# Kernel tuning notes

Measured on AMD Instinct MI355X. Metric: run time of the kernel, lower is better.

Reference implementation:

```python
import jax, jax.numpy as jnp
import numpy as np
import math

B = 2; SEQ = 4096; D_MODEL = 768; D_STATE = 128; D_CONV = 4; EXPAND = 2; HEAD_DIM = 64
D_INNER = EXPAND * D_MODEL; D_SSM = D_INNER; NH = D_SSM // HEAD_DIM  # 24 heads
CONV_DIM = D_SSM + 2 * D_STATE; CHUNK = 256
D_IN_PROJ = 2 * D_INNER + 2 * D_STATE + NH


def causal_conv1d(x, w, b):
    # x: [B, C, L]; w: [C, W] depthwise kernel; left-pad for causality; silu activation
    W = w.shape[-1]; L = x.shape[-1]
    xp = jnp.pad(x, ((0, 0), (0, 0), (W - 1, 0)))
    y = b[None, :, None] + sum(xp[:, :, k:k + L] * w[None, :, k, None] for k in range(W))
    return jax.nn.silu(y)


def segsum(a):
    # a: [..., S] -> [..., S, S]; entry (i,j) = sum_{k=j+1..i} a_k for i>=j, -inf above diag
    S = a.shape[-1]
    cs = jnp.cumsum(a, -1)
    d = cs[..., :, None] - cs[..., None, :]
    mask = jnp.tril(jnp.ones((S, S), bool))
    return jnp.where(mask, d, -jnp.inf)


def ssd_chunk_scan(x, dt, A, Bm, Cm, Dp, chunk):
    # Mamba2 SSD chunked selective scan. x:[b,l,h,p] dt:[b,l,h] A:[h] Bm,Cm:[b,l,n] Dp:[h]
    b, l, h, p = x.shape; n = Bm.shape[-1]; nc = l // chunk
    xc = x.reshape(b, nc, chunk, h, p)
    Bc = Bm.reshape(b, nc, chunk, n)
    Cc = Cm.reshape(b, nc, chunk, n)
    dtc = dt.reshape(b, nc, chunk, h)
    a = jnp.transpose(A[None, None, None, :] * dtc, (0, 3, 1, 2))  # [b,h,c,s]
    Acs = jnp.cumsum(a, -1)
    Lm = jnp.exp(segsum(a))  # [b,h,c,s,s] lower-triangular decay
    # intra-chunk (diagonal block) outputs
    Ydiag = jnp.einsum('bcsn,bczn,bhcsz,bczh,bczhp->bcshp', Cc, Bc, Lm, dtc, xc)
    # per-chunk end states
    decay_states = jnp.exp(Acs[..., -1:] - Acs)  # [b,h,c,s]
    states = jnp.einsum('bczn,bhcz,bczh,bczhp->bchpn', Bc, decay_states, dtc, xc)
    # inter-chunk recurrence over nc chunks (small) via scan
    decay_chunk = jnp.exp(Acs[..., -1])  # [b,h,c]
    def step(hcar, inp):
        dcy, st = inp
        return dcy[..., None, None] * hcar + st, hcar  # emit state entering chunk
    _, prev = jax.lax.scan(step, jnp.zeros_like(states[:, 0]),
                           (jnp.moveaxis(decay_chunk, -1, 0), jnp.moveaxis(states, 1, 0)))
    prev = jnp.moveaxis(prev, 0, 1)  # [b,c,h,p,n]
    Yoff = jnp.einsum('bcsn,bchpn,bhcs->bcshp', Cc, prev, jnp.exp(Acs))
    return (Ydiag + Yoff).reshape(b, l, h, p) + Dp[None, None, :, None] * x


def _forward(u, time_diff, W_in, b_in, conv_w, conv_b, tconv1_w, tconv1_b,
             tconv2_w, tconv2_b, mlp_w1, mlp_b1, mlp_w2, mlp_b2, gate_w, gate_b,
             ln_w, ln_b, A_log, dt_bias, Dp, norm_w, W_out, b_out):
    silu = jax.nn.silu
    zxbcdt = u @ W_in.T + b_in  # [B,L,d_in_proj], d_mlp=0
    z = zxbcdt[..., :D_SSM]
    xBC = zxbcdt[..., D_SSM:D_SSM + CONV_DIM]
    dt = zxbcdt[..., D_SSM + CONV_DIM:]  # [B,L,H]
    A = -jnp.exp(A_log)
    xBC = jnp.transpose(causal_conv1d(jnp.transpose(xBC, (0, 2, 1)), conv_w, conv_b), (0, 2, 1))
    # time-gated dt path (time_diff: [B,H,L])
    ts = silu(time_diff @ mlp_w1.T + mlp_b1) @ mlp_w2.T + mlp_b2
    tdt = ts * time_diff
    tdt = causal_conv1d(tdt, tconv1_w, tconv1_b)
    tdt = causal_conv1d(tdt, tconv2_w, tconv2_b)  # [B,H,L]
    final_dt = dt * jnp.transpose(tdt, (0, 2, 1))
    x = xBC[..., :D_SSM]
    Bm = xBC[..., D_SSM:D_SSM + D_STATE]
    Cm = xBC[..., D_SSM + D_STATE:]
    dt_sp = jax.nn.softplus(final_dt + dt_bias)
    xh = x.reshape(x.shape[0], x.shape[1], NH, HEAD_DIM)
    y = ssd_chunk_scan(xh, dt_sp, A, Bm, Cm, Dp, CHUNK).reshape(x.shape[0], x.shape[1], D_SSM)
    # gated RMSNorm (norm_before_gate=False): gate first, then normalize
    yg = y * silu(z)
    y = yg * jax.lax.rsqrt(jnp.mean(yg * yg, -1, keepdims=True) + 1e-12) * norm_w
    out = y @ W_out.T + b_out
    # time residual gate + LayerNorm over seq_len
    tg = jax.nn.sigmoid(time_diff @ gate_w.T + gate_b)  # [B,H,1]
    tmix = tg * time_diff + (1.0 - tg) * tdt
    mu = jnp.mean(tmix, -1, keepdims=True)
    var = jnp.mean((tmix - mu) ** 2, -1, keepdims=True)
    time_out = (tmix - mu) * jax.lax.rsqrt(var + 1e-12) * ln_w + ln_b
    return out, time_out


def setup_inputs():
    key = jax.random.key(0)
    ks = jax.random.split(key, 16)
    def nrm(k, shape, scale=0.02):
        return jax.random.normal(k, shape, jnp.float32) * scale
    dtv = jnp.exp(jax.random.uniform(ks[10], (NH,), jnp.float32) * (math.log(0.1) - math.log(0.001)) + math.log(0.001))
    dtv = jnp.clip(dtv, 1e-4)
    dt_bias = dtv + jnp.log(-jnp.expm1(-dtv))
    A_log = jnp.log(jax.random.uniform(ks[11], (NH,), jnp.float32, 1.0, 16.0))
    return dict(
        u=jax.random.normal(ks[0], (B, SEQ, D_MODEL), jnp.float32),
        time_diff=jax.random.uniform(ks[1], (B, NH, SEQ), jnp.float32),
        W_in=nrm(ks[2], (D_IN_PROJ, D_MODEL)), b_in=jnp.zeros((D_IN_PROJ,), jnp.float32),
        conv_w=nrm(ks[3], (CONV_DIM, D_CONV), 0.2), conv_b=jnp.zeros((CONV_DIM,), jnp.float32),
        tconv1_w=nrm(ks[4], (NH, D_CONV), 0.2), tconv1_b=jnp.zeros((NH,), jnp.float32),
        tconv2_w=nrm(ks[5], (NH, D_CONV), 0.2), tconv2_b=jnp.zeros((NH,), jnp.float32),
        mlp_w1=nrm(ks[6], (SEQ, SEQ)), mlp_b1=jnp.zeros((SEQ,), jnp.float32),
        mlp_w2=nrm(ks[7], (SEQ, SEQ)), mlp_b2=jnp.zeros((SEQ,), jnp.float32),
        gate_w=nrm(ks[8], (1, SEQ)), gate_b=jnp.zeros((1,), jnp.float32),
        ln_w=jnp.ones((SEQ,), jnp.float32), ln_b=jnp.zeros((SEQ,), jnp.float32),
        A_log=A_log, dt_bias=dt_bias, Dp=jnp.ones((NH,), jnp.float32),
        norm_w=jnp.ones((D_SSM,), jnp.float32),
        W_out=nrm(ks[9], (D_MODEL, D_INNER)), b_out=jnp.zeros((D_MODEL,), jnp.float32),
    )


def reference(u, time_diff, W_in, b_in, conv_w, conv_b, tconv1_w, tconv1_b,
              tconv2_w, tconv2_b, mlp_w1, mlp_b1, mlp_w2, mlp_b2, gate_w, gate_b,
              ln_w, ln_b, A_log, dt_bias, Dp, norm_w, W_out, b_out):
    return _forward(u, time_diff, W_in, b_in, conv_w, conv_b, tconv1_w, tconv1_b,
                    tconv2_w, tconv2_b, mlp_w1, mlp_b1, mlp_w2, mlp_b2, gate_w, gate_b,
                    ln_w, ln_b, A_log, dt_bias, Dp, norm_w, W_out, b_out)
```

## Files before the change

kernel.cpp:

```cpp
#include <hip/hip_runtime.h>
#include <math.h>

#define BB 2
#define SEQ 4096
#define DMODEL 768
#define DSTATE 128
#define NHH 24
#define HDIM 64
#define DSSM 1536
#define CDIM 1792
#define CHK 256
#define NC 16
#define DPROJ 3352
#define MR (BB*SEQ)
#define KSPLIT 32
#define XSTR 1920
#define CT 16
#define SXS 270
#define STS 134

typedef __attribute__((ext_vector_type(8))) short bf16x8;
typedef __attribute__((ext_vector_type(8))) unsigned short u16x8;
typedef __attribute__((ext_vector_type(4))) float f32x4;

__device__ __forceinline__ float siluf(float x) { return x / (1.0f + expf(-x)); }

__device__ __forceinline__ unsigned short f2bf(float f) {
    unsigned u = __float_as_uint(f);
    unsigned r = (u + 0x7fffu + ((u >> 16) & 1u)) >> 16;
    return (unsigned short)r;
}

__device__ __forceinline__ float bf2f(unsigned short u) {
    return __uint_as_float(((unsigned)u) << 16);
}

__device__ __forceinline__ float4 bf2f4(ushort4 v) {
    float4 o;
    o.x = bf2f(v.x); o.y = bf2f(v.y); o.z = bf2f(v.z); o.w = bf2f(v.w);
    return o;
}

__device__ __forceinline__ bf16x8 pack8(float4 a, float4 b) {
    u16x8 r;
    r[0] = f2bf(a.x); r[1] = f2bf(a.y); r[2] = f2bf(a.z); r[3] = f2bf(a.w);
    r[4] = f2bf(b.x); r[5] = f2bf(b.y); r[6] = f2bf(b.z); r[7] = f2bf(b.w);
    return *(bf16x8*)&r;
}

__device__ __forceinline__ void gload_lds16(const void* g, void* l) {
    __builtin_amdgcn_global_load_lds((const __attribute__((address_space(1))) unsigned int*)g,
                                     (__attribute__((address_space(3))) unsigned int*)l, 16, 0, 0);
}

__global__ __launch_bounds__(256) void cvt_bf16_k(const float* __restrict__ in,
    unsigned short* __restrict__ out, int n_valid, int n_total)
{
    int i = (blockIdx.x * 256 + threadIdx.x) * 4;
    if (i >= n_total) return;
    ushort4 o;
    if (i + 3 < n_valid) {
        float4 v = *(const float4*)&in[i];
        o.x = f2bf(v.x); o.y = f2bf(v.y); o.z = f2bf(v.z); o.w = f2bf(v.w);
    } else {
        o.x = (i + 0 < n_valid) ? f2bf(in[i + 0]) : 0;
        o.y = (i + 1 < n_valid) ? f2bf(in[i + 1]) : 0;
        o.z = (i + 2 < n_valid) ? f2bf(in[i + 2]) : 0;
        o.w = (i + 3 < n_valid) ? f2bf(in[i + 3]) : 0;
    }
    *(ushort4*)&out[i] = o;
}

__global__ __launch_bounds__(256) void gemm_dual_skinny(
    const unsigned short* __restrict__ A,
    const unsigned short* __restrict__ B1, const float* __restrict__ bias1,
    unsigned short* __restrict__ C1, int N1, int NT1, int nbias1, int NWG1,
    const unsigned short* __restrict__ B2, const float* __restrict__ bias2,
    unsigned short* __restrict__ C2, int N2, int NT2, int nbias2,
    int K, int KT, int NWGD,
    const float* __restrict__ skA, const float* __restrict__ skB,
    float* __restrict__ skPart, int skN, int skK)
{
    __shared__ unsigned short SMEM[24576];
    const int tid = threadIdx.x;
    const int w = tid >> 6, l = tid & 63;
    const int lr = l & 15, lk = l >> 4;
    int nwg = gridDim.x, bid = blockIdx.x;
    int wg = (nwg & 7) ? bid : ((bid & 7) * (nwg >> 3) + (bid >> 3));
    if (wg >= NWGD) {
        int t = wg - NWGD;
        int nb = t & 31, kb = t >> 5;
        const int n0s = nb * 128;
        const int KS = skK / KSPLIT;
        const int k0 = kb * KS;
        const int nw0 = n0s + w * 32;
        f32x4 sacc[3][2] = {};
        for (int kt = 0; kt < KS; kt += 32) {
            int kk = k0 + kt + lk * 8;
            bf16x8 af[3], bfr[2];
#pragma unroll
            for (int mi = 0; mi < 3; ++mi) {
                const float* ap = &skA[(size_t)(mi * 16 + lr) * skK + kk];
                af[mi] = pack8(*(const float4*)ap, *(const float4*)(ap + 4));
            }
#pragma unroll
            for (int nf = 0; nf < 2; ++nf) {
                const float* bp = &skB[(size_t)(nw0 + nf * 16 + lr) * skK + kk];
                bfr[nf] = pack8(*(const float4*)bp, *(const float4*)(bp + 4));
            }
#pragma unroll
            for (int mi = 0; mi < 3; ++mi)
#pragma unroll
                for (int nf = 0; nf < 2; ++nf)
                    sacc[mi][nf] = __builtin_amdgcn_mfma_f32_16x16x32_bf16(af[mi], bfr[nf], sacc[mi][nf], 0, 0, 0);
        }
        float* pb = skPart + (size_t)kb * 48 * skN;
#pragma unroll
        for (int mi = 0; mi < 3; ++mi)
#pragma unroll
            for (int r = 0; r < 4; ++r)
#pragma unroll
                for (int nf = 0; nf < 2; ++nf)
                    pb[(size_t)(mi * 16 + lk * 4 + r) * skN + nw0 + nf * 16 + lr] = sacc[mi][nf][r];
        return;
    }
    const int wr = w >> 1, wc = w & 1;
    const int lkx = lk ^ ((lr >> 1) & 3);
    const unsigned short* B;
    const float* bias;
    unsigned short* C;
    int N, NT, nbias;
    if (wg < NWG1) { B = B1; bias = bias1; C = C1; N = N1; NT = NT1; nbias = nbias1; }
    else { wg -= NWG1; B = B2; bias = bias2; C = C2; N = N2; NT = NT2; nbias = nbias2; }
    const int m0 = (wg / NT) * 128, n0 = (wg % NT) * 128;
    f32x4 acc[4][4] = {};
    const int i16 = w * 64 + l;
    const int row0 = i16 >> 2, sl = i16 & 3;
    const int slx = sl ^ ((row0 >> 1) & 3);
    const size_t ga0 = (size_t)(m0 + row0) * K + slx * 8;
    const size_t ga1 = (size_t)(m0 + row0 + 64) * K + slx * 8;
    const size_t gb0 = (size_t)(n0 + row0) * K + slx * 8;
    const size_t gb1 = (size_t)(n0 + row0 + 64) * K + slx * 8;
    const int lo0 = (w * 64) * 8;
    const int lo1 = (256 + w * 64) * 8;

#define STAGE(bb, kt) { int ko = (kt) * 32; int bs = (bb) * 8192;            \
      gload_lds16(A + ga0 + ko, &SMEM[bs + lo0]);                            \
      gload_lds16(A + ga1 + ko, &SMEM[bs + lo1]);                            \
      gload_lds16(B + gb0 + ko, &SMEM[bs + 4096 + lo0]);                     \
      gload_lds16(B + gb1 + ko, &SMEM[bs + 4096 + lo1]); }

    STAGE(0, 0);
    STAGE(1, 1);
    for (int kt = 0; kt < KT; ++kt) {
        if (kt + 1 < KT) {
            asm volatile("s_waitcnt vmcnt(4)" ::: "memory");
        } else {
            asm volatile("s_waitcnt vmcnt(0)" ::: "memory");
        }
        __builtin_amdgcn_s_barrier();
        if (kt + 2 < KT) STAGE((kt + 2) % 3, kt + 2);
        int bs = (kt % 3) * 8192;
        bf16x8 af[4], bg[4];
#pragma unroll
        for (int mi = 0; mi < 4; ++mi)
            af[mi] = *(const bf16x8*)&SMEM[bs + (wr * 64 + mi * 16 + lr) * 32 + lkx * 8];
#pragma unroll
        for (int nj = 0; nj < 4; ++nj)
            bg[nj] = *(const bf16x8*)&SMEM[bs + 4096 + (wc * 64 + nj * 16 + lr) * 32 + lkx * 8];
#pragma unroll
        for (int mi = 0; mi < 4; ++mi)
#pragma unroll
            for (int nj = 0; nj < 4; ++nj)
                acc[mi][nj] = __builtin_amdgcn_mfma_f32_16x16x32_bf16(af[mi], bg[nj], acc[mi][nj], 0, 0, 0);
    }
#undef STAGE
    {
        unsigned short* CL = SMEM;
#pragma unroll
        for (int half = 0; half < 2; ++half) {
            __syncthreads();
            if (wr == half) {
#pragma unroll
                for (int nj = 0; nj < 4; ++nj) {
                    int col = n0 + wc * 64 + nj * 16 + lr;
                    float bz = (col < nbias) ? bias[col] : 0.f;
                    int cl = wc * 64 + nj * 16 + lr;
#pragma unroll
                    for (int mi = 0; mi < 4; ++mi)
#pragma unroll
                        for (int r = 0; r < 4; ++r)
                            CL[(mi * 16 + lk * 4 + r) * 136 + cl] = f2bf(acc[mi][nj][r] + bz);
                }
            }
            __syncthreads();
            for (int i = tid; i < 1024; i += 256) {
                int rr = i >> 4, c8 = (i & 15) * 8;
                int m = m0 + half * 64 + rr;
                *(u16x8*)&C[(size_t)m * N + n0 + c8] = *(const u16x8*)&CL[rr * 136 + c8];
            }
        }
    }
}

__global__ __launch_bounds__(256) void conv_skinny2_k(const unsigned short* __restrict__ xbc,
    const float* __restrict__ cw, const float* __restrict__ cb,
    unsigned short* __restrict__ out,
    const float* __restrict__ skA, const float* __restrict__ skB,
    float* __restrict__ skPart, int skN, int skK, int NWGC)
{
    int bid = blockIdx.x;
    int tid = threadIdx.x;
    if (bid >= NWGC) {
        int t = bid - NWGC;
        int nb = t & 31, kb = t >> 5;
        const int n0s = nb * 128;
        const int KS = skK / KSPLIT;
        const int k0 = kb * KS;
        const int w = tid >> 6, l = tid & 63;
        const int lr = l & 15, lk = l >> 4;
        const int nw0 = n0s + w * 32;
        f32x4 sacc[3][2] = {};
        for (int kt = 0; kt < KS; kt += 32) {
            int kk = k0 + kt + lk * 8;
            bf16x8 af[3], bfr[2];
#pragma unroll
            for (int mi = 0; mi < 3; ++mi) {
                const float* ap = &skA[(size_t)(mi * 16 + lr) * skK + kk];
                af[mi] = pack8(*(const float4*)ap, *(const float4*)(ap + 4));
            }
#pragma unroll
            for (int nf = 0; nf < 2; ++nf) {
                const float* bp = &skB[(size_t)(nw0 + nf * 16 + lr) * skK + kk];
                bfr[nf] = pack8(*(const float4*)bp, *(const float4*)(bp + 4));
            }
#pragma unroll
            for (int mi = 0; mi < 3; ++mi)
#pragma unroll
                for (int nf = 0; nf < 2; ++nf)
                    sacc[mi][nf] = __builtin_amdgcn_mfma_f32_16x16x32_bf16(af[mi], bfr[nf], sacc[mi][nf], 0, 0, 0);
        }
        float* pb = skPart + (size_t)kb * 48 * skN;
#pragma unroll
        for (int mi = 0; mi < 3; ++mi)
#pragma unroll
            for (int r = 0; r < 4; ++r)
#pragma unroll
                for (int nf = 0; nf < 2; ++nf)
                    pb[(size_t)(mi * 16 + lk * 4 + r) * skN + nw0 + nf * 16 + lr] = sacc[mi][nf][r];
        return;
    }
    int idx = bid * 256 + tid;
    int slot = idx % 448;
    int g = idx / 448;
    int c4 = slot * 4;
    int b = g / (SEQ / CT);
    int t0 = (g % (SEQ / CT)) * CT;
    size_t rb = (size_t)b * SEQ;
    float4 cw0 = *(const float4*)&cw[(c4 + 0) * 4];
    float4 cw1 = *(const float4*)&cw[(c4 + 1) * 4];
    float4 cw2 = *(const float4*)&cw[(c4 + 2) * 4];
    float4 cw3 = *(const float4*)&cw[(c4 + 3) * 4];
    float4 cbv = *(const float4*)&cb[c4];
    float4 zero = {0.f, 0.f, 0.f, 0.f};
    float4 w0, w1, w2;
    w0 = (t0 - 3 >= 0) ? bf2f4(*(const ushort4*)&xbc[(rb + t0 - 3) * XSTR + c4]) : zero;
    w1 = (t0 - 2 >= 0) ? bf2f4(*(const ushort4*)&xbc[(rb + t0 - 2) * XSTR + c4]) : zero;
    w2 = (t0 - 1 >= 0) ? bf2f4(*(const ushort4*)&xbc[(rb + t0 - 1) * XSTR + c4]) : zero;
#pragma unroll
    for (int i = 0; i < CT; ++i) {
        int t = t0 + i;
        float4 w3 = bf2f4(*(const ushort4*)&xbc[(rb + t) * XSTR + c4]);
        float a0 = cbv.x + w0.x * cw0.x + w1.x * cw0.y + w2.x * cw0.z + w3.x * cw0.w;
        float a1 = cbv.y + w0.y * cw1.x + w1.y * cw1.y + w2.y * cw1.z + w3.y * cw1.w;
        float a2 = cbv.z + w0.z * cw2.x + w1.z * cw2.y + w2.z * cw2.z + w3.z * cw2.w;
        float a3 = cbv.w + w0.w * cw3.x + w1.w * cw3.y + w2.w * cw3.z + w3.w * cw3.w;
        ushort4 o;
        o.x = f2bf(siluf(a0)); o.y = f2bf(siluf(a1));
        o.z = f2bf(siluf(a2)); o.w = f2bf(siluf(a3));
        *(ushort4*)&out[(rb + t) * CDIM + c4] = o;
        w0 = w1; w1 = w2; w2 = w3;
    }
}

__global__ __launch_bounds__(256) void reduce_part_k(const float* __restrict__ part,
    const float* __restrict__ bias, float* __restrict__ out, int N, int act)
{
    int idx = blockIdx.x * 256 + threadIdx.x;
    if (idx >= 48 * N) return;
    int n = idx % N;
    float s = bias[n];
#pragma unroll
    for (int kb = 0; kb < KSPLIT; ++kb) s += part[(size_t)kb * 48 * N + idx];
    if (act) s = siluf(s);
    out[idx] = s;
}

__global__ __launch_bounds__(256) void time_conv_k(const float* __restrict__ ts,
    const float* __restrict__ td, const float* __restrict__ w1, const float* __restrict__ b1,
    const float* __restrict__ w2, const float* __restrict__ b2, float* __restrict__ tdt)
{
    __shared__ float u0[SEQ];
    __shared__ float u1[SEQ];
    int row = blockIdx.x, h = row % NHH;
    const float* tsr = ts + (size_t)row * SEQ;
    const float* tdr = td + (size_t)row * SEQ;
    for (int i = threadIdx.x; i < SEQ; i += 256) u0[i] = tsr[i] * tdr[i];
    __syncthreads();
    float wa[4], wb[4];
#pragma unroll
    for (int k = 0; k < 4; ++k) { wa[k] = w1[h * 4 + k]; wb[k] = w2[h * 4 + k]; }
    float ba = b1[h], bbv = b2[h];
    for (int i = threadIdx.x; i < SEQ; i += 256) {
        float acc = ba;
#pragma unroll
        for (int k = 0; k < 4; ++k) { int tt = i + k - 3; if (tt >= 0) acc = fmaf(u0[tt], wa[k], acc); }
        u1[i] = siluf(acc);
    }
    __syncthreads();
    for (int i = threadIdx.x; i < SEQ; i += 256) {
        float acc = bbv;
#pragma unroll
        for (int k = 0; k < 4; ++k) { int tt = i + k - 3; if (tt >= 0) acc = fmaf(u1[tt], wb[k], acc); }
        tdt[(size_t)row * SEQ + i] = siluf(acc);
    }
}

__global__ __launch_bounds__(256) void dtsp_cum_k(const unsigned short* __restrict__ r1,
    const float* __restrict__ tdt, const float* __restrict__ dt_bias,
    const float* __restrict__ A_log, float* __restrict__ dtp, float* __restrict__ acs)
{
    __shared__ float wsum[4];
    int blk = blockIdx.x;
    int c = blk % NC;
    int bh = blk / NC;
    int h = bh % NHH, b = bh / NHH;
    int tid = threadIdx.x;
    int s = c * CHK + tid;
    size_t base = (size_t)bh * SEQ + s;
    float x = bf2f(r1[((size_t)(b * SEQ + s)) * XSTR + CDIM + h]) * tdt[base] + dt_bias[h];
    float dt = (x > 20.0f) ? x : log1pf(expf(x));
    dtp[base] = dt;
    float Ah = -expf(A_log[h]);
    float v = Ah * dt;
    int ln = tid & 63;
#pragma unroll
    for (int off = 1; off < 64; off <<= 1) {
        float t = __shfl_up(v, off, 64);
        if (ln >= off) v += t;
    }
    if (ln == 63) wsum[tid >> 6] = v;
    __syncthreads();
    float add = 0.f;
    int wv = tid >> 6;
#pragma unroll
    for (int i = 0; i < 3; ++i)
        if (i < wv) add += wsum[i];
    acs[base] = v + add;
}

__global__ __launch_bounds__(256) void ssd_states_sraw_k(const unsigned short* __restrict__ xc,
    const float* __restrict__ dtp, const float* __restrict__ acs_g,
    float* __restrict__ st, unsigned short* __restrict__ sraw)
{
    __shared__ float s_coef[256];
    __shared__ unsigned short SXT[64 * STS];
    __shared__ unsigned short SBT[128 * STS];
    int bid = blockIdx.x;
    int blk = (gridDim.x & 7) ? bid : ((bid & 7) * (gridDim.x >> 3) + (bid >> 3));
    int tid = threadIdx.x;
    int w = tid >> 6, l = tid & 63;
    int lr = l & 15, lk = l >> 4;
    if (blk >= BB * NC * NHH) {
        int t = blk - BB * NC * NHH;
        int bc = t / 10, tile = t % 10;
        int rem = tile, st_i = 0;
        for (st_i = 0; ; ++st_i) { if (rem < st_i + 1) break; rem -= st_i + 1; }
        int zt = rem;
        int b = bc / NC, c = bc % NC;
        size_t rowbase = (size_t)b * SEQ + c * CHK;
        for (int i = tid; i < 64 * 32; i += 256) {
            int r = i >> 5, c4 = (i & 31) * 4;
            *(ushort4*)&SXT[r * STS + c4] = *(const ushort4*)&xc[(rowbase + st_i * 64 + r) * CDIM + DSSM + DSTATE + c4];
            *(ushort4*)&SBT[r * STS + c4] = *(const ushort4*)&xc[(rowbase + zt * 64 + r) * CDIM + DSSM + c4];
        }
        __syncthreads();
        f32x4 d[4] = {};
#pragma unroll
        for (int kt = 0; kt < 4; ++kt) {
            bf16x8 av = *(const bf16x8*)&SXT[(w * 16 + lr) * STS + kt * 32 + lk * 8];
            bf16x8 bv[4];
#pragma unroll
            for (int nj = 0; nj < 4; ++nj)
                bv[nj] = *(const bf16x8*)&SBT[(nj * 16 + lr) * STS + kt * 32 + lk * 8];
#pragma unroll
            for (int nj = 0; nj < 4; ++nj)
                d[nj] = __builtin_amdgcn_mfma_f32_16x16x32_bf16(av, bv[nj], d[nj], 0, 0, 0);
        }
        unsigned short* tp = sraw + (size_t)bc * 16 * 4096 + (size_t)(st_i * 4 + zt) * 4096;
#pragma unroll
        for (int nj = 0; nj < 4; ++nj)
#pragma unroll
            for (int r = 0; r < 4; ++r)
                tp[(w * 16 + lk * 4 + r) * 64 + nj * 16 + lr] = f2bf(d[nj][r]);
        return;
    }
    int h = blk % NHH, c = (blk / NHH) % NC, b = blk / (NHH * NC);
    size_t rowbase = (size_t)b * SEQ + c * CHK;
    size_t dbase = (size_t)(b * NHH + h) * SEQ + c * CHK;
    float alv = acs_g[dbase + 255];
    s_coef[tid] = expf(alv - acs_g[dbase + tid]) * dtp[dbase + tid];
    __syncthreads();
    f32x4 acc[4][2] = {};
    for (int z0 = 0; z0 < CHK; z0 += 128) {
        if (z0) __syncthreads();
        for (int i = tid; i < 128 * 8; i += 256) {
            int zz = i >> 3, p8 = (i & 7) * 8;
            float sc = s_coef[z0 + zz];
            u16x8 v = *(const u16x8*)&xc[(rowbase + z0 + zz) * CDIM + h * HDIM + p8];
#pragma unroll
            for (int e = 0; e < 8; ++e)
                SXT[(p8 + e) * STS + zz] = f2bf(bf2f(v[e]) * sc);
        }
        for (int i = tid; i < 128 * 16; i += 256) {
            int zz = i >> 4, n8 = (i & 15) * 8;
            u16x8 v = *(const u16x8*)&xc[(rowbase + z0 + zz) * CDIM + DSSM + n8];
#pragma unroll
            for (int e = 0; e < 8; ++e)
                SBT[(n8 + e) * STS + zz] = v[e];
        }
        __syncthreads();
#pragma unroll
        for (int kt = 0; kt < 4; ++kt) {
            bf16x8 av[4], bv[2];
#pragma unroll
            for (int mi = 0; mi < 4; ++mi)
                av[mi] = *(const bf16x8*)&SXT[(mi * 16 + lr) * STS + kt * 32 + lk * 8];
#pragma unroll
            for (int nj = 0; nj < 2; ++nj)
                bv[nj] = *(const bf16x8*)&SBT[(w * 32 + nj * 16 + lr) * STS + kt * 32 + lk * 8];
#pragma unroll
            for (int mi = 0; mi < 4; ++mi)
#pragma unroll
                for (int nj = 0; nj < 2; ++nj)
                    acc[mi][nj] = __builtin_amdgcn_mfma_f32_16x16x32_bf16(av[mi], bv[nj], acc[mi][nj], 0, 0, 0);
        }
    }
    size_t base = (size_t)blk * (HDIM * DSTATE);
#pragma unroll
    for (int mi = 0; mi < 4; ++mi)
#pragma unroll
        for (int r = 0; r < 4; ++r) {
            int p = mi * 16 + lk * 4 + r;
#pragma unroll
            for (int nj = 0; nj < 2; ++nj)
                st[base + p * DSTATE + w * 32 + nj * 16 + lr] = acc[mi][nj][r];
        }
}

__global__ __launch_bounds__(256) void ssd_scan_k(const float* __restrict__ st,
    const float* __restrict__ acs_g, unsigned short* __restrict__ pv16)
{
    int b = blockIdx.x / NHH, h = blockIdx.x % NHH;
    int tid = threadIdx.x;
    float carry[32];
#pragma unroll
    for (int j = 0; j < 32; ++j) carry[j] = 0.f;
    for (int c = 0; c < NC; ++c) {
        int bch = (b * NC + c) * NHH + h;
        size_t base = (size_t)bch * (HDIM * DSTATE);
        float dcy = expf(acs_g[(size_t)(b * NHH + h) * SEQ + c * CHK + 255]);
#pragma unroll
        for (int j = 0; j < 32; ++j) {
            pv16[base + tid + j * 256] = f2bf(carry[j]);
            carry[j] = fmaf(dcy, carry[j], st[base + tid + j * 256]);
        }
    }
}

__global__ __launch_bounds__(256) void ssd_y2_k(const unsigned short* __restrict__ xc,
    const float* __restrict__ dtp, const float* __restrict__ acs_g,
    const unsigned short* __restrict__ sraw, const unsigned short* __restrict__ pv16,
    const float* __restrict__ Dp, unsigned short* __restrict__ Ybf)
{
    __shared__ unsigned short SXT[32 * SXS];
    int bid = blockIdx.x;
    int blk2 = (gridDim.x & 7) ? bid : ((bid & 7) * (gridDim.x >> 3) + (bid >> 3));
    int half = blk2 & 1;
    int blk = blk2 >> 1;
    int h = blk % NHH;
    int c = (blk / NHH) % NC;
    int b = blk / (NHH * NC);
    int tid = threadIdx.x;
    int w = tid >> 6, l = tid & 63;
    int lr = l & 15, lk = l >> 4;
    int pbase = half * 32;
    size_t rowbase = (size_t)b * SEQ + c * CHK;
    size_t dbase = (size_t)(b * NHH + h) * SEQ + c * CHK;
    for (int i = tid; i < 256 * 4; i += 256) {
        int z = i >> 2, p8 = (i & 3) * 8;
        float az0q = acs_g[dbase + (z & 192)];
        float e = az0q - acs_g[dbase + z];
        if (e > 60.f) e = 60.f;
        float sc = expf(e) * dtp[dbase + z];
        u16x8 v = *(const u16x8*)&xc[(rowbase + z) * CDIM + h * HDIM + pbase + p8];
#pragma unroll
        for (int e2 = 0; e2 < 8; ++e2)
            SXT[(p8 + e2) * SXS + z] = f2bf(bf2f(v[e2]) * sc);
    }
    float az0w = acs_g[dbase + w * 64];
    float esw[4][4];
#pragma unroll
    for (int mi = 0; mi < 4; ++mi)
#pragma unroll
        for (int r = 0; r < 4; ++r)
            esw[mi][r] = expf(acs_g[dbase + w * 64 + mi * 16 + lk * 4 + r] - az0w);
    __syncthreads();

    const unsigned short* tbase = sraw + (size_t)(b * NC + c) * 16 * 4096;
    const unsigned short* pvbase = pv16 + (size_t)blk * (HDIM * DSTATE);
    f32x4 acc[4][2] = {};
    for (int zt = 0; zt < w; ++zt) {
        const unsigned short* tp = tbase + (size_t)(w * 4 + zt) * 4096;
        f32x4 tmp[4][2] = {};
#pragma unroll
        for (int kt = 0; kt < 2; ++kt) {
            bf16x8 av[4], bv[2];
#pragma unroll
            for (int mi = 0; mi < 4; ++mi)
                av[mi] = *(const bf16x8*)&tp[(mi * 16 + lr) * 64 + kt * 32 + lk * 8];
#pragma unroll
            for (int nj = 0; nj < 2; ++nj)
                bv[nj] = *(const bf16x8*)&SXT[(nj * 16 + lr) * SXS + zt * 64 + kt * 32 + lk * 8];
#pragma unroll
            for (int mi = 0; mi < 4; ++mi)
#pragma unroll
                for (int nj = 0; nj < 2; ++nj)
                    tmp[mi][nj] = __builtin_amdgcn_mfma_f32_16x16x32_bf16(av[mi], bv[nj], tmp[mi][nj], 0, 0, 0);
        }
        float rho = expf(az0w - acs_g[dbase + zt * 64]);
#pragma unroll
        for (int mi = 0; mi < 4; ++mi)
#pragma unroll
            for (int r = 0; r < 4; ++r) {
                float es = esw[mi][r] * rho;
#pragma unroll
                for (int nj = 0; nj < 2; ++nj)
                    acc[mi][nj][r] += es * tmp[mi][nj][r];
            }
    }
    {
        const unsigned short* tp = tbase + (size_t)(w * 4 + w) * 4096;
        f32x4 tmp[4][2] = {};
#pragma unroll
        for (int kt = 0; kt < 2; ++kt) {
            bf16x8 av[4], bv[2];
#pragma unroll
            for (int mi = 0; mi < 4; ++mi) {
                av[mi] = *(const bf16x8*)&tp[(mi * 16 + lr) * 64 + kt * 32 + lk * 8];
                int zb = kt * 32 + lk * 8;
                int sl = mi * 16 + lr;
#pragma unroll
                for (int e = 0; e < 8; ++e)
                    if (zb + e > sl) av[mi][e] = 0;
            }
#pragma unroll
            for (int nj = 0; nj < 2; ++nj)
                bv[nj] = *(const bf16x8*)&SXT[(nj * 16 + lr) * SXS + w * 64 + kt * 32 + lk * 8];
#pragma unroll
            for (int mi = 0; mi < 4; ++mi)
#pragma unroll
                for (int nj = 0; nj < 2; ++nj)
                    tmp[mi][nj] = __builtin_amdgcn_mfma_f32_16x16x32_bf16(av[mi], bv[nj], tmp[mi][nj], 0, 0, 0);
        }
#pragma unroll
        for (int mi = 0; mi < 4; ++mi)
#pragma unroll
            for (int r = 0; r < 4; ++r) {
                float es = esw[mi][r];
#pragma unroll
                for (int nj = 0; nj < 2; ++nj)
                    acc[mi][nj][r] += es * tmp[mi][nj][r];
            }
    }
    {
        f32x4 tmp[4][2] = {};
#pragma unroll
        for (int kt = 0; kt < 4; ++kt) {
            bf16x8 av[4], bv[2];
#pragma unroll
            for (int mi = 0; mi < 4; ++mi)
                av[mi] = *(const bf16x8*)&xc[(rowbase + w * 64 + mi * 16 + lr) * CDIM + DSSM + DSTATE + kt * 32 + lk * 8];
#pragma unroll
            for (int nj = 0; nj < 2; ++nj)
                bv[nj] = *(const bf16x8*)&pvbase[(pbase + nj * 16 + lr) * DSTATE + kt * 32 + lk * 8];
#pragma unroll
            for (int mi = 0; mi < 4; ++mi)
#pragma unroll
                for (int nj = 0; nj < 2; ++nj)
                    tmp[mi][nj] = __builtin_amdgcn_mfma_f32_16x16x32_bf16(av[mi], bv[nj], tmp[mi][nj], 0, 0, 0);
        }
        float eoff = expf(az0w);
#pragma unroll
        for (int mi = 0; mi < 4; ++mi)
#pragma unroll
            for (int r = 0; r < 4; ++r) {
                float es = esw[mi][r] * eoff;
#pragma unroll
                for (int nj = 0; nj < 2; ++nj)
                    acc[mi][nj][r] += es * tmp[mi][nj][r];
            }
    }
    float dph = Dp[h];
#pragma unroll
    for (int mi = 0; mi < 4; ++mi) {
#pragma unroll
        for (int r = 0; r < 4; ++r) {
            int s = w * 64 + mi * 16 + lk * 4 + r;
#pragma unroll
            for (int nj = 0; nj < 2; ++nj) {
                int p = pbase + nj * 16 + lr;
                float xv = bf2f(xc[(rowbase + s) * CDIM + h * HDIM + p]);
                Ybf[(rowbase + s) * DSSM + h * HDIM + p] = f2bf(acc[mi][nj][r] + dph * xv);
            }
        }
    }
}

__global__ __launch_bounds__(256) void rmsnorm_k(const unsigned short* __restrict__ Ybf_in,
    const unsigned short* __restrict__ zbf, const float* __restrict__ nw,
    unsigned short* __restrict__ Ybf_out)
{
    __shared__ float red[8];
    int row = blockIdx.x;
    const unsigned short* y = Ybf_in + (size_t)row * DSSM;
    const unsigned short* z = zbf + (size_t)row * DSSM;
    float v[6];
    float ss = 0.f;
#pragma unroll
    for (int k = 0; k < 6; ++k) {
        int i = threadIdx.x + k * 256;
        float g = bf2f(y[i]) * siluf(bf2f(z[i]));
        v[k] = g;
        ss = fmaf(g, g, ss);
    }
#pragma unroll
    for (int o = 32; o > 0; o >>= 1) ss += __shfl_down(ss, o, 64);
    int wv = threadIdx.x >> 6, ln = threadIdx.x & 63;
    if (ln == 0) red[wv] = ss;
    __syncthreads();
    float tot = red[0] + red[1] + red[2] + red[3];
    float sc = rsqrtf(tot / (float)DSSM + 1e-12f);
    unsigned short* yo = Ybf_out + (size_t)row * DSSM;
#pragma unroll
    for (int k = 0; k < 6; ++k) {
        int i = threadIdx.x + k * 256;
        yo[i] = f2bf(v[k] * sc * nw[i]);
    }
}

__global__ __launch_bounds__(256) void gemm_out_timeout_k(
    const unsigned short* __restrict__ A, const unsigned short* __restrict__ B,
    const float* __restrict__ bias, float* __restrict__ C, int N, int K, int KT, int NT, int NWGG,
    const float* __restrict__ td, const float* __restrict__ tdt,
    const float* __restrict__ gw, const float* __restrict__ gb,
    const float* __restrict__ lnw, const float* __restrict__ lnb, float* __restrict__ out2)
{
    __shared__ __align__(16) unsigned char SMEMRAW[49152];
    unsigned short* SMEM = (unsigned short*)SMEMRAW;
    const int tid = threadIdx.x;
    int nwg = gridDim.x, bid = blockIdx.x;
    int wg = (nwg & 7) ? bid : ((bid & 7) * (nwg >> 3) + (bid >> 3));
    if (wg >= NWGG) {
        float* tm = (float*)SMEMRAW;
        __shared__ float red[8];
        int row = wg - NWGG;
        const float* tdr = td + (size_t)row * SEQ;
        const float* tdtr = tdt + (size_t)row * SEQ;
        int wv = tid >> 6, ln = tid & 63;
        float part = 0.f;
        for (int i = tid; i < SEQ; i += 256) part = fmaf(tdr[i], gw[i], part);
#pragma unroll
        for (int o = 32; o > 0; o >>= 1) part += __shfl_down(part, o, 64);
        if (ln == 0) red[wv] = part;
        __syncthreads();
        float dot = red[0] + red[1] + red[2] + red[3];
        float tg = 1.f / (1.f + expf(-(dot + gb[0])));
        __syncthreads();
        float sum = 0.f;
        for (int i = tid; i < SEQ; i += 256) {
            float x = tg * tdr[i] + (1.f - tg) * tdtr[i];
            tm[i] = x;
            sum += x;
        }
#pragma unroll
        for (int o = 32; o > 0; o >>= 1) sum += __shfl_down(sum, o, 64);
        if (ln == 0) red[wv] = sum;
        __syncthreads();
        float mu = (red[0] + red[1] + red[2] + red[3]) / (float)SEQ;
        __syncthreads();
        float s2 = 0.f;
        for (int i = tid; i < SEQ; i += 256) { float d = tm[i] - mu; s2 = fmaf(d, d, s2); }
#pragma unroll
        for (int o = 32; o > 0; o >>= 1) s2 += __shfl_down(s2, o, 64);
        if (ln == 0) red[wv] = s2;
        __syncthreads();
        float var = (red[0] + red[1] + red[2] + red[3]) / (float)SEQ;
        float inv = rsqrtf(var + 1e-12f);
        for (int i = tid; i < SEQ; i += 256)
            out2[(size_t)row * SEQ + i] = (tm[i] - mu) * inv * lnw[i] + lnb[i];
        return;
    }
    const int w = tid >> 6, l = tid & 63;
    const int wr = w >> 1, wc = w & 1;
    const int lr = l & 15, lk = l >> 4;
    const int lkx = lk ^ ((lr >> 1) & 3);
    const int m0 = (wg / NT) * 128, n0 = (wg % NT) * 128;
    f32x4 acc[4][4] = {};
    const int i16 = w * 64 + l;
    const int row0 = i16 >> 2, sl = i16 & 3;
    const int slx = sl ^ ((row0 >> 1) & 3);
    const size_t ga0 = (size_t)(m0 + row0) * K + slx * 8;
    const size_t ga1 = (size_t)(m0 + row0 + 64) * K + slx * 8;
    const size_t gb0 = (size_t)(n0 + row0) * K + slx * 8;
    const size_t gb1 = (size_t)(n0 + row0 + 64) * K + slx * 8;
    const int lo0 = (w * 64) * 8;
    const int lo1 = (256 + w * 64) * 8;

#define STAGE3(bb, kt) { int ko = (kt) * 32; int bs = (bb) * 8192;           \
      gload_lds16(A + ga0 + ko, &SMEM[bs + lo0]);                            \
      gload_lds16(A + ga1 + ko, &SMEM[bs + lo1]);                            \
      gload_lds16(B + gb0 + ko, &SMEM[bs + 4096 + lo0]);                     \
      gload_lds16(B + gb1 + ko, &SMEM[bs + 4096 + lo1]); }

    STAGE3(0, 0);
    STAGE3(1, 1);
    for (int kt = 0; kt < KT; ++kt) {
        if (kt + 1 < KT) {
            asm volatile("s_waitcnt vmcnt(4)" ::: "memory");
        } else {
            asm volatile("s_waitcnt vmcnt(0)" ::: "memory");
        }
        __builtin_amdgcn_s_barrier();
        if (kt + 2 < KT) STAGE3((kt + 2) % 3, kt + 2);
        int bs = (kt % 3) * 8192;
        bf16x8 af[4], bg[4];
#pragma unroll
        for (int mi = 0; mi < 4; ++mi)
            af[mi] = *(const bf16x8*)&SMEM[bs + (wr * 64 + mi * 16 + lr) * 32 + lkx * 8];
#pragma unroll
        for (int nj = 0; nj < 4; ++nj)
            bg[nj] = *(const bf16x8*)&SMEM[bs + 4096 + (wc * 64 + nj * 16 + lr) * 32 + lkx * 8];
#pragma unroll
        for (int mi = 0; mi < 4; ++mi)
#pragma unroll
            for (int nj = 0; nj < 4; ++nj)
                acc[mi][nj] = __builtin_amdgcn_mfma_f32_16x16x32_bf16(af[mi], bg[nj], acc[mi][nj], 0, 0, 0);
    }
#undef STAGE3
#pragma unroll
    for (int nj = 0; nj < 4; ++nj) {
        int col = n0 + wc * 64 + nj * 16 + lr;
        float bz = bias[col];
#pragma unroll
        for (int mi = 0; mi < 4; ++mi) {
#pragma unroll
            for (int r = 0; r < 4; ++r) {
                int m = m0 + wr * 64 + mi * 16 + lk * 4 + r;
                C[(size_t)m * N + col] = acc[mi][nj][r] + bz;
            }
        }
    }
}

extern "C" void kernel_launch(void* const* d_in, const int* in_sizes, int n_in,
                              void* d_out, int out_size, void* d_ws, size_t ws_size,
                              hipStream_t stream)
{
    const float* u      = (const float*)d_in[0];
    const float* td     = (const float*)d_in[1];
    const float* W_in   = (const float*)d_in[2];
    const float* b_in   = (const float*)d_in[3];
    const float* conv_w = (const float*)d_in[4];
    const float* conv_b = (const float*)d_in[5];
    const float* t1w    = (const float*)d_in[6];
    const float* t1b    = (const float*)d_in[7];
    const float* t2w    = (const float*)d_in[8];
    const float* t2b    = (const float*)d_in[9];
    const float* m1w    = (const float*)d_in[10];
    const float* m1b    = (const float*)d_in[11];
    const float* m2w    = (const float*)d_in[12];
    const float* m2b    = (const float*)d_in[13];
    const float* gw     = (const float*)d_in[14];
    const float* gb     = (const float*)d_in[15];
    const float* lnw    = (const float*)d_in[16];
    const float* lnb    = (const float*)d_in[17];
    const float* A_log  = (const float*)d_in[18];
    const float* dt_bias= (const float*)d_in[19];
    const float* Dpv    = (const float*)d_in[20];
    const float* nw     = (const float*)d_in[21];
    const float* W_out  = (const float*)d_in[22];
    const float* b_out  = (const float*)d_in[23];
    float* out  = (float*)d_out;
    float* out2 = out + (size_t)MR * DMODEL;

    float* ws = (float*)d_ws;
    size_t o = 0;
    float* zbuf  = ws + o; o += (size_t)MR * DSSM;
    float* r1    = ws + o; o += (size_t)MR * DSSM;
    float* xcv   = ws + o; o += (size_t)MR * CDIM / 2;
    float* partb = ws + o; o += (size_t)KSPLIT * 48 * SEQ;
    float* hid   = ws + o; o += (size_t)BB * NHH * SEQ;
    float* tss   = ws + o; o += (size_t)BB * NHH * SEQ;
    float* tdt   = ws + o; o += (size_t)BB * NHH * SEQ;
    float* dtp   = ws + o; o += (size_t)MR * NHH;
    float* acs_g = ws + o; o += (size_t)MR * NHH;
    float* pvb   = ws + o; o += (size_t)BB * NC * NHH * HDIM * DSTATE;
    unsigned short* sraw = (unsigned short*)(ws + o); o += (size_t)BB * NC * 16 * 4096 / 2;
    unsigned short* r1b = (unsigned short*)r1;
    float* stb = r1;
    unsigned short* ybf16 = (unsigned short*)r1;
    unsigned short* xcv_bf = (unsigned short*)xcv;
    unsigned short* u_bf  = (unsigned short*)pvb;
    unsigned short* Wi_bf = (unsigned short*)(pvb + 3145728);
    unsigned short* pv16  = (unsigned short*)pvb;
    unsigned short* zbf   = (unsigned short*)zbuf;
    unsigned short* Y_bf  = (unsigned short*)xcv;
    unsigned short* Wo_bf = (unsigned short*)(zbuf + 6291456);

    dim3 blk(256);
    const int NWG1 = (XSTR / 128) * (MR / 128);
    const int NWGD = NWG1 + (DSSM / 128) * (MR / 128);
    const int NWGSK = (SEQ / 128) * KSPLIT;
    const int NWGC = 448 * (MR / CT) / 256;

    cvt_bf16_k<<<dim3((MR * DMODEL / 4 + 255) / 256), blk, 0, stream>>>(u, u_bf, MR * DMODEL, MR * DMODEL);
    cvt_bf16_k<<<dim3((3456 * DMODEL / 4 + 255) / 256), blk, 0, stream>>>(W_in, Wi_bf, DPROJ * DMODEL, 3456 * DMODEL);
    cvt_bf16_k<<<dim3((DMODEL * DSSM / 4 + 255) / 256), blk, 0, stream>>>(W_out, Wo_bf, DMODEL * DSSM, DMODEL * DSSM);
    gemm_dual_skinny<<<dim3(NWGD + NWGSK), blk, 0, stream>>>(
        u_bf,
        Wi_bf + (size_t)DSSM * DMODEL, b_in + DSSM, r1b, XSTR, XSTR / 128, DPROJ - DSSM, NWG1,
        Wi_bf, b_in, zbf, DSSM, DSSM / 128, DSSM,
        DMODEL, DMODEL / 32, NWGD,
        td, m1w, partb, SEQ, SEQ);
    reduce_part_k<<<dim3((48 * SEQ + 255) / 256), blk, 0, stream>>>(partb, m1b, hid, SEQ, 1);
    conv_skinny2_k<<<dim3(NWGC + NWGSK), blk, 0, stream>>>(
        r1b, conv_w, conv_b, xcv_bf, hid, m2w, partb, SEQ, SEQ, NWGC);
    reduce_part_k<<<dim3((48 * SEQ + 255) / 256), blk, 0, stream>>>(partb, m2b, tss, SEQ, 0);
    time_conv_k<<<dim3(BB * NHH), blk, 0, stream>>>(tss, td, t1w, t1b, t2w, t2b, tdt);
    dtsp_cum_k<<<dim3(BB * NHH * NC), blk, 0, stream>>>(r1b, tdt, dt_bias, A_log, dtp, acs_g);
    ssd_states_sraw_k<<<dim3(BB * NC * NHH + BB * NC * 10), blk, 0, stream>>>(xcv_bf, dtp, acs_g, stb, sraw);
    ssd_scan_k<<<dim3(BB * NHH), blk, 0, stream>>>(stb, acs_g, pv16);
    ssd_y2_k<<<dim3(BB * NC * NHH * 2), blk, 0, stream>>>(xcv_bf, dtp, acs_g, sraw, pv16, Dpv, ybf16);
    rmsnorm_k<<<dim3(MR), blk, 0, stream>>>(ybf16, zbf, nw, Y_bf);
    gemm_out_timeout_k<<<dim3((DMODEL / 128) * (MR / 128) + BB * NHH), blk, 0, stream>>>(
        Y_bf, Wo_bf, b_out, out, DMODEL, DSSM, DSSM / 32, DMODEL / 128, (DMODEL / 128) * (MR / 128),
        td, tdt, gw, gb, lnw, lnb, out2);
}
```

Measured before the change: 325.8 us.

## Enlarge in-projection GEMM tile to 256x128 with 512-thread workgroups

Doubles the M extent of each in-projection GEMM workgroup to 256 rows with 8 waves, so each B tile staged in LDS is reused by twice as many rows. This cuts global B traffic and halves the number of GEMM workgroups. The fused skinny split-K path now runs 8 waves per 128 columns, each covering 16 columns instead of 32. The trade-offs are more LDS per workgroup, fewer workgroups to spread across CUs, and a single-pass epilogue that needs a 256-row LDS staging buffer.

```diff
diff --git a/kernel.cpp b/kernel.cpp
--- a/kernel.cpp
+++ b/kernel.cpp
@@ -71,7 +71,7 @@
     *(ushort4*)&out[i] = o;
 }
 
-__global__ __launch_bounds__(256) void gemm_dual_skinny(
+__global__ __launch_bounds__(512) void gemm_dual_skinny(
     const unsigned short* __restrict__ A,
     const unsigned short* __restrict__ B1, const float* __restrict__ bias1,
     unsigned short* __restrict__ C1, int N1, int NT1, int nbias1, int NWG1,
@@ -81,7 +81,7 @@
     const float* __restrict__ skA, const float* __restrict__ skB,
     float* __restrict__ skPart, int skN, int skK)
 {
-    __shared__ unsigned short SMEM[24576];
+    __shared__ unsigned short SMEM[36864];
     const int tid = threadIdx.x;
     const int w = tid >> 6, l = tid & 63;
     const int lr = l & 15, lk = l >> 4;
@@ -93,35 +93,30 @@
         const int n0s = nb * 128;
         const int KS = skK / KSPLIT;
         const int k0 = kb * KS;
-        const int nw0 = n0s + w * 32;
-        f32x4 sacc[3][2] = {};
+        const int nw0 = n0s + w * 16;
+        f32x4 sacc[3] = {};
         for (int kt = 0; kt < KS; kt += 32) {
             int kk = k0 + kt + lk * 8;
-            bf16x8 af[3], bfr[2];
+            bf16x8 af[3], bfr;
 #pragma unroll
             for (int mi = 0; mi < 3; ++mi) {
                 const float* ap = &skA[(size_t)(mi * 16 + lr) * skK + kk];
                 af[mi] = pack8(*(const float4*)ap, *(const float4*)(ap + 4));
             }
-#pragma unroll
-            for (int nf = 0; nf < 2; ++nf) {
-                const float* bp = &skB[(size_t)(nw0 + nf * 16 + lr) * skK + kk];
-                bfr[nf] = pack8(*(const float4*)bp, *(const float4*)(bp + 4));
+            {
+                const float* bp = &skB[(size_t)(nw0 + lr) * skK + kk];
+                bfr = pack8(*(const float4*)bp, *(const float4*)(bp + 4));
             }
 #pragma unroll
             for (int mi = 0; mi < 3; ++mi)
-#pragma unroll
-                for (int nf = 0; nf < 2; ++nf)
-                    sacc[mi][nf] = __builtin_amdgcn_mfma_f32_16x16x32_bf16(af[mi], bfr[nf], sacc[mi][nf], 0, 0, 0);
+                sacc[mi] = __builtin_amdgcn_mfma_f32_16x16x32_bf16(af[mi], bfr, sacc[mi], 0, 0, 0);
         }
         float* pb = skPart + (size_t)kb * 48 * skN;
 #pragma unroll
         for (int mi = 0; mi < 3; ++mi)
 #pragma unroll
             for (int r = 0; r < 4; ++r)
-#pragma unroll
-                for (int nf = 0; nf < 2; ++nf)
-                    pb[(size_t)(mi * 16 + lk * 4 + r) * skN + nw0 + nf * 16 + lr] = sacc[mi][nf][r];
+                pb[(size_t)(mi * 16 + lk * 4 + r) * skN + nw0 + lr] = sacc[mi][r];
         return;
     }
     const int wr = w >> 1, wc = w & 1;
@@ -132,42 +127,38 @@
     int N, NT, nbias;
     if (wg < NWG1) { B = B1; bias = bias1; C = C1; N = N1; NT = NT1; nbias = nbias1; }
     else { wg -= NWG1; B = B2; bias = bias2; C = C2; N = N2; NT = NT2; nbias = nbias2; }
-    const int m0 = (wg / NT) * 128, n0 = (wg % NT) * 128;
+    const int m0 = (wg / NT) * 256, n0 = (wg % NT) * 128;
     f32x4 acc[4][4] = {};
-    const int i16 = w * 64 + l;
-    const int row0 = i16 >> 2, sl = i16 & 3;
+    const int row0 = tid >> 2, sl = tid & 3;
     const int slx = sl ^ ((row0 >> 1) & 3);
     const size_t ga0 = (size_t)(m0 + row0) * K + slx * 8;
-    const size_t ga1 = (size_t)(m0 + row0 + 64) * K + slx * 8;
+    const size_t ga1 = (size_t)(m0 + row0 + 128) * K + slx * 8;
     const size_t gb0 = (size_t)(n0 + row0) * K + slx * 8;
-    const size_t gb1 = (size_t)(n0 + row0 + 64) * K + slx * 8;
-    const int lo0 = (w * 64) * 8;
-    const int lo1 = (256 + w * 64) * 8;
-
-#define STAGE(bb, kt) { int ko = (kt) * 32; int bs = (bb) * 8192;            \
+    const int lo0 = tid * 8;
+
+#define STAGE(bb, kt) { int ko = (kt) * 32; int bs = (bb) * 12288;           \
       gload_lds16(A + ga0 + ko, &SMEM[bs + lo0]);                            \
-      gload_lds16(A + ga1 + ko, &SMEM[bs + lo1]);                            \
-      gload_lds16(B + gb0 + ko, &SMEM[bs + 4096 + lo0]);                     \
-      gload_lds16(B + gb1 + ko, &SMEM[bs + 4096 + lo1]); }
+      gload_lds16(A + ga1 + ko, &SMEM[bs + 4096 + lo0]);                     \
+      gload_lds16(B + gb0 + ko, &SMEM[bs + 8192 + lo0]); }
 
     STAGE(0, 0);
     STAGE(1, 1);
     for (int kt = 0; kt < KT; ++kt) {
         if (kt + 1 < KT) {
-            asm volatile("s_waitcnt vmcnt(4)" ::: "memory");
+            asm volatile("s_waitcnt vmcnt(3)" ::: "memory");
         } else {
             asm volatile("s_waitcnt vmcnt(0)" ::: "memory");
         }
         __builtin_amdgcn_s_barrier();
         if (kt + 2 < KT) STAGE((kt + 2) % 3, kt + 2);
-        int bs = (kt % 3) * 8192;
+        int bs = (kt % 3) * 12288;
         bf16x8 af[4], bg[4];
 #pragma unroll
         for (int mi = 0; mi < 4; ++mi)
             af[mi] = *(const bf16x8*)&SMEM[bs + (wr * 64 + mi * 16 + lr) * 32 + lkx * 8];
 #pragma unroll
         for (int nj = 0; nj < 4; ++nj)
-            bg[nj] = *(const bf16x8*)&SMEM[bs + 4096 + (wc * 64 + nj * 16 + lr) * 32 + lkx * 8];
+            bg[nj] = *(const bf16x8*)&SMEM[bs + 8192 + (wc * 64 + nj * 16 + lr) * 32 + lkx * 8];
 #pragma unroll
         for (int mi = 0; mi < 4; ++mi)
 #pragma unroll
@@ -177,28 +168,22 @@
 #undef STAGE
     {
         unsigned short* CL = SMEM;
-#pragma unroll
-        for (int half = 0; half < 2; ++half) {
-            __syncthreads();
-            if (wr == half) {
-#pragma unroll
-                for (int nj = 0; nj < 4; ++nj) {
-                    int col = n0 + wc * 64 + nj * 16 + lr;
-                    float bz = (col < nbias) ? bias[col] : 0.f;
-                    int cl = wc * 64 + nj * 16 + lr;
-#pragma unroll
-                    for (int mi = 0; mi < 4; ++mi)
-#pragma unroll
-                        for (int r = 0; r < 4; ++r)
-                            CL[(mi * 16 + lk * 4 + r) * 136 + cl] = f2bf(acc[mi][nj][r] + bz);
-                }
-            }
-            __syncthreads();
-            for (int i = tid; i < 1024; i += 256) {
-                int rr = i >> 4, c8 = (i & 15) * 8;
-                int m = m0 + half * 64 + rr;
-                *(u16x8*)&C[(size_t)m * N + n0 + c8] = *(const u16x8*)&CL[rr * 136 + c8];
-            }
+        __syncthreads();
+#pragma unroll
+        for (int nj = 0; nj < 4; ++nj) {
+            int col = n0 + wc * 64 + nj * 16 + lr;
+            float bz = (col < nbias) ? bias[col] : 0.f;
+            int cl = wc * 64 + nj * 16 + lr;
+#pragma unroll
+            for (int mi = 0; mi < 4; ++mi)
+#pragma unroll
+                for (int r = 0; r < 4; ++r)
+                    CL[(wr * 64 + mi * 16 + lk * 4 + r) * 136 + cl] = f2bf(acc[mi][nj][r] + bz);
+        }
+        __syncthreads();
+        for (int i = tid; i < 4096; i += 512) {
+            int rr = i >> 4, c8 = (i & 15) * 8;
+            *(u16x8*)&C[(size_t)(m0 + rr) * N + n0 + c8] = *(const u16x8*)&CL[rr * 136 + c8];
         }
     }
 }
@@ -828,16 +813,16 @@
     unsigned short* Y_bf  = (unsigned short*)xcv;
     unsigned short* Wo_bf = (unsigned short*)(zbuf + 6291456);
 
-    dim3 blk(256);
-    const int NWG1 = (XSTR / 128) * (MR / 128);
-    const int NWGD = NWG1 + (DSSM / 128) * (MR / 128);
+    dim3 blk(256), blk512(512);
+    const int NWG1 = (XSTR / 128) * (MR / 256);
+    const int NWGD = NWG1 + (DSSM / 128) * (MR / 256);
     const int NWGSK = (SEQ / 128) * KSPLIT;
     const int NWGC = 448 * (MR / CT) / 256;
 
     cvt_bf16_k<<<dim3((MR * DMODEL / 4 + 255) / 256), blk, 0, stream>>>(u, u_bf, MR * DMODEL, MR * DMODEL);
     cvt_bf16_k<<<dim3((3456 * DMODEL / 4 + 255) / 256), blk, 0, stream>>>(W_in, Wi_bf, DPROJ * DMODEL, 3456 * DMODEL);
     cvt_bf16_k<<<dim3((DMODEL * DSSM / 4 + 255) / 256), blk, 0, stream>>>(W_out, Wo_bf, DMODEL * DSSM, DMODEL * DSSM);
-    gemm_dual_skinny<<<dim3(NWGD + NWGSK), blk, 0, stream>>>(
+    gemm_dual_skinny<<<dim3(NWGD + NWGSK), blk512, 0, stream>>>(
         u_bf,
         Wi_bf + (size_t)DSSM * DMODEL, b_in + DSSM, r1b, XSTR, XSTR / 128, DPROJ - DSSM, NWG1,
         Wi_bf, b_in, zbf, DSSM, DSSM / 128, DSSM,
```

Result: slower. 348.0 us (+6.8%).
